# Performance work log

Hardware: AMD Instinct MI355X
Metric: run time of the kernel (lower is better)

Reference implementation:

```python
import jax, jax.numpy as jnp
import numpy as np

DIM = 96
HEADS = 3
HEAD_DIM = DIM // HEADS
WIN = (4, 4, 4)
N_WIN = WIN[0] * WIN[1] * WIN[2]  # 64 tokens per window
HIDDEN = int(DIM * 4.0)
EPS = 1e-5


def setup_inputs() -> dict:
    key = jax.random.key(0)
    ks = jax.random.split(key, 16)
    s = lambda fan: 1.0 / np.sqrt(fan)
    return {
        "x": jax.random.normal(ks[0], (1, 64, 96, 96, 96), jnp.float32),
        "g1": jnp.ones((DIM,), jnp.float32),
        "b1": jnp.zeros((DIM,), jnp.float32),
        "wq": jax.random.normal(ks[1], (DIM, DIM), jnp.float32) * s(DIM),
        "bq": jnp.zeros((DIM,), jnp.float32),
        "wkv": jax.random.normal(ks[2], (DIM, 2 * DIM), jnp.float32) * s(DIM),
        "bkv": jnp.zeros((2 * DIM,), jnp.float32),
        "wp": jax.random.normal(ks[3], (DIM, DIM), jnp.float32) * s(DIM),
        "bp": jnp.zeros((DIM,), jnp.float32),
        "g2": jnp.ones((DIM,), jnp.float32),
        "b2": jnp.zeros((DIM,), jnp.float32),
        "w1": jax.random.normal(ks[4], (DIM, HIDDEN), jnp.float32) * s(DIM),
        "bm1": jnp.zeros((HIDDEN,), jnp.float32),
        "w2": jax.random.normal(ks[5], (HIDDEN, DIM), jnp.float32) * s(HIDDEN),
        "bm2": jnp.zeros((DIM,), jnp.float32),
    }


def _layernorm(x, g, b):
    mu = jnp.mean(x, axis=-1, keepdims=True)
    var = jnp.mean(jnp.square(x - mu), axis=-1, keepdims=True)
    return (x - mu) * jax.lax.rsqrt(var + EPS) * g + b


def _window_partition(x):
    B, D, H, W, C = x.shape
    wd, wh, ww = WIN
    x = x.reshape(B, D // wd, wd, H // wh, wh, W // ww, ww, C)
    x = x.transpose(0, 1, 3, 5, 2, 4, 6, 7)
    return x.reshape(-1, N_WIN, C)


def _window_reverse(win, B, D, H, W):
    wd, wh, ww = WIN
    C = win.shape[-1]
    x = win.reshape(B, D // wd, H // wh, W // ww, wd, wh, ww, C)
    x = x.transpose(0, 1, 4, 2, 5, 3, 6, 7)
    return x.reshape(B, D, H, W, C)


def reference(x, g1, b1, wq, bq, wkv, bkv, wp, bp, g2, b2, w1, bm1, w2, bm2):
    B, D, H, W, C = x.shape
    # --- part 1: LN -> window attention -> residual ---
    h = _layernorm(x, g1, b1)
    # D,H,W chosen divisible by window size, so padding is a no-op
    xw = _window_partition(h)                       # (nW, N, C)
    nW = xw.shape[0]
    q = (xw @ wq + bq).reshape(nW, N_WIN, HEADS, HEAD_DIM)
    kv = (xw @ wkv + bkv).reshape(nW, N_WIN, 2, HEADS, HEAD_DIM)
    k, v = kv[:, :, 0], kv[:, :, 1]                 # (nW, N, h, hd)
    scale = HEAD_DIM ** -0.5
    attn = jnp.einsum("wnhd,wmhd->whnm", q * scale, k)
    attn = jax.nn.softmax(attn, axis=-1)
    out = jnp.einsum("whnm,wmhd->wnhd", attn, v).reshape(nW, N_WIN, C)
    out = out @ wp + bp
    attn_out = _window_reverse(out, B, D, H, W)
    x = x + attn_out
    # --- part 2: LN -> MLP -> residual ---
    h2 = _layernorm(x, g2, b2)
    h2 = jax.nn.gelu(h2 @ w1 + bm1, approximate=False) @ w2 + bm2
    return x + h2
```

## Files before the change

kernel.cpp:

```cpp
#include <hip/hip_runtime.h>

typedef __bf16 bf16x8 __attribute__((ext_vector_type(8)));
typedef __bf16 bf16x4 __attribute__((ext_vector_type(4)));
typedef float f32x4 __attribute__((ext_vector_type(4)));

#define MFMA(a,b,c) __builtin_amdgcn_mfma_f32_16x16x32_bf16(a, b, c, 0, 0, 0)

__device__ __forceinline__ float gelu_f(float t) {
    float t2 = t * t;
    float m = t * __builtin_fmaf(-0.07135481627f, t2, -1.5957691216f);
    float e = __expf(m);
    return t * __builtin_amdgcn_rcpf(1.0f + e);
}

__global__ void prep_weights(const float* __restrict__ wq, const float* __restrict__ wkv,
                             const float* __restrict__ wp, const float* __restrict__ w1,
                             const float* __restrict__ w2, __bf16* __restrict__ ws) {
    int i = blockIdx.x * 256 + threadIdx.x;
    const float scale = 0.17677669529663687f;
    if (i < 9216) {
        int n = i / 96, k = i % 96;
        ws[i] = (__bf16)(wq[k * 96 + n] * scale);
    } else if (i < 27648) {
        int j = i - 9216; int n = j / 96, k = j % 96;
        ws[i] = (__bf16)(wkv[k * 192 + n]);
    } else if (i < 36864) {
        int j = i - 27648; int n = j / 96, k = j % 96;
        ws[i] = (__bf16)(wp[k * 96 + n]);
    } else if (i < 73728) {
        int j = i - 36864; int n = j / 96, k = j % 96;
        ws[i] = (__bf16)(w1[k * 384 + n]);
    } else if (i < 110592) {
        int j = i - 73728; int n = j / 384, k = j % 384;
        ws[i] = (__bf16)(w2[k * 96 + n]);
    }
}

#define LDH 104

__global__ __launch_bounds__(256, 2) void attn_kernel(
    const float* __restrict__ x, const float* __restrict__ g1v, const float* __restrict__ b1v,
    const float* __restrict__ bq, const float* __restrict__ bkv, const float* __restrict__ bp,
    const __bf16* __restrict__ ws, float* __restrict__ xmid)
{
    const __bf16* wqt  = ws;
    const __bf16* wkvt = ws + 9216;
    const __bf16* wpt  = ws + 27648;

    __shared__ __align__(16) __bf16 h_lds[64 * LDH];
    __shared__ __align__(16) __bf16 q_lds[64 * LDH];
    __shared__ __align__(16) __bf16 k_lds[64 * LDH];
    __shared__ __align__(16) __bf16 vt_lds[96 * 72];
    __shared__ __align__(16) __bf16 p_lds[4 * 16 * 72];

    const int tid = threadIdx.x;
    const int wv = tid >> 6, lane = tid & 63;
    const int c = lane & 15, g = lane >> 4;
    const int mp = wv >> 1, ng = wv & 1;

    const int wid = blockIdx.x;
    const int wdI = wid / 576, rem = wid % 576, whI = rem / 24, wwI = rem % 24;
    const int tok = tid >> 2, cseg = (tid & 3) * 24;
    const int dz = tok >> 4, hy = (tok >> 2) & 3, wx = tok & 3;
    const long gbase = (((long)(wdI * 4 + dz) * 96 + (whI * 4 + hy)) * 96 + (wwI * 4 + wx)) * 96 + cseg;

    float xr[24];
    #pragma unroll
    for (int j = 0; j < 6; ++j) {
        float4 v = *reinterpret_cast<const float4*>(x + gbase + j * 4);
        xr[j*4+0] = v.x; xr[j*4+1] = v.y; xr[j*4+2] = v.z; xr[j*4+3] = v.w;
    }
    float s = 0.f;
    #pragma unroll
    for (int j = 0; j < 24; ++j) s += xr[j];
    s += __shfl_xor(s, 1); s += __shfl_xor(s, 2);
    float mu = s * (1.0f / 96.0f);
    float vs = 0.f;
    #pragma unroll
    for (int j = 0; j < 24; ++j) { float d = xr[j] - mu; vs += d * d; }
    vs += __shfl_xor(vs, 1); vs += __shfl_xor(vs, 2);
    float rstd = rsqrtf(vs * (1.0f / 96.0f) + 1e-5f);
    #pragma unroll
    for (int j = 0; j < 6; ++j) {
        float4 gv = *reinterpret_cast<const float4*>(g1v + cseg + j * 4);
        float4 bv = *reinterpret_cast<const float4*>(b1v + cseg + j * 4);
        h_lds[tok * LDH + cseg + j*4+0] = (__bf16)((xr[j*4+0] - mu) * rstd * gv.x + bv.x);
        h_lds[tok * LDH + cseg + j*4+1] = (__bf16)((xr[j*4+1] - mu) * rstd * gv.y + bv.y);
        h_lds[tok * LDH + cseg + j*4+2] = (__bf16)((xr[j*4+2] - mu) * rstd * gv.z + bv.z);
        h_lds[tok * LDH + cseg + j*4+3] = (__bf16)((xr[j*4+3] - mu) * rstd * gv.w + bv.w);
    }
    __syncthreads();

    {
        f32x4 acc[2][3];
        #pragma unroll
        for (int mi = 0; mi < 2; ++mi)
            #pragma unroll
            for (int nl = 0; nl < 3; ++nl) acc[mi][nl] = (f32x4){0.f, 0.f, 0.f, 0.f};
        #pragma unroll
        for (int kc = 0; kc < 3; ++kc) {
            bf16x8 a[2];
            #pragma unroll
            for (int mi = 0; mi < 2; ++mi)
                a[mi] = *reinterpret_cast<const bf16x8*>(&h_lds[((mp*2+mi)*16 + c) * LDH + kc*32 + g*8]);
            #pragma unroll
            for (int nl = 0; nl < 3; ++nl) {
                int nt = ng * 3 + nl;
                bf16x8 b = *reinterpret_cast<const bf16x8*>(&wqt[(nt*16 + c) * 96 + kc*32 + g*8]);
                #pragma unroll
                for (int mi = 0; mi < 2; ++mi)
                    acc[mi][nl] = MFMA(a[mi], b, acc[mi][nl]);
            }
        }
        #pragma unroll
        for (int nl = 0; nl < 3; ++nl) {
            int n = (ng * 3 + nl) * 16 + c;
            float bias = bq[n] * 0.17677669529663687f;
            #pragma unroll
            for (int mi = 0; mi < 2; ++mi)
                #pragma unroll
                for (int r = 0; r < 4; ++r)
                    q_lds[((mp*2+mi)*16 + g*4 + r) * LDH + n] = (__bf16)(acc[mi][nl][r] + bias);
        }
    }

    {
        f32x4 acc[4][3];
        #pragma unroll
        for (int m = 0; m < 4; ++m)
            #pragma unroll
            for (int nl = 0; nl < 3; ++nl) acc[m][nl] = (f32x4){0.f, 0.f, 0.f, 0.f};
        #pragma unroll
        for (int kc = 0; kc < 3; ++kc) {
            bf16x8 a[4];
            #pragma unroll
            for (int m = 0; m < 4; ++m)
                a[m] = *reinterpret_cast<const bf16x8*>(&h_lds[(m*16 + c) * LDH + kc*32 + g*8]);
            #pragma unroll
            for (int nl = 0; nl < 3; ++nl) {
                int nt = wv * 3 + nl;
                bf16x8 b = *reinterpret_cast<const bf16x8*>(&wkvt[(nt*16 + c) * 96 + kc*32 + g*8]);
                #pragma unroll
                for (int m = 0; m < 4; ++m)
                    acc[m][nl] = MFMA(a[m], b, acc[m][nl]);
            }
        }
        #pragma unroll
        for (int nl = 0; nl < 3; ++nl) {
            int n = (wv * 3 + nl) * 16 + c;
            float bias = bkv[n];
            if (wv < 2) {
                #pragma unroll
                for (int m = 0; m < 4; ++m)
                    #pragma unroll
                    for (int r = 0; r < 4; ++r)
                        k_lds[(m*16 + g*4 + r) * LDH + n] = (__bf16)(acc[m][nl][r] + bias);
            } else {
                int nv = n - 96;
                #pragma unroll
                for (int m = 0; m < 4; ++m) {
                    bf16x4 pk;
                    pk.x = (__bf16)(acc[m][nl][0] + bias);
                    pk.y = (__bf16)(acc[m][nl][1] + bias);
                    pk.z = (__bf16)(acc[m][nl][2] + bias);
                    pk.w = (__bf16)(acc[m][nl][3] + bias);
                    *reinterpret_cast<bf16x4*>(&vt_lds[nv * 72 + m*16 + g*4]) = pk;
                }
            }
        }
    }
    __syncthreads();

    __bf16* p_w = &p_lds[wv * (16 * 72)];
    #pragma unroll
    for (int h = 0; h < 3; ++h) {
        f32x4 sacc[4];
        #pragma unroll
        for (int nt = 0; nt < 4; ++nt) sacc[nt] = (f32x4){0.f, 0.f, 0.f, 0.f};
        bf16x8 a = *reinterpret_cast<const bf16x8*>(&q_lds[(wv*16 + c) * LDH + h*32 + g*8]);
        #pragma unroll
        for (int nt = 0; nt < 4; ++nt) {
            bf16x8 b = *reinterpret_cast<const bf16x8*>(&k_lds[(nt*16 + c) * LDH + h*32 + g*8]);
            sacc[nt] = MFMA(a, b, sacc[nt]);
        }
        float mx[4];
        #pragma unroll
        for (int r = 0; r < 4; ++r) {
            float m0 = fmaxf(fmaxf(sacc[0][r], sacc[1][r]), fmaxf(sacc[2][r], sacc[3][r]));
            m0 = fmaxf(m0, __shfl_xor(m0, 1));
            m0 = fmaxf(m0, __shfl_xor(m0, 2));
            m0 = fmaxf(m0, __shfl_xor(m0, 4));
            m0 = fmaxf(m0, __shfl_xor(m0, 8));
            mx[r] = m0;
        }
        float p[4][4];
        #pragma unroll
        for (int nt = 0; nt < 4; ++nt)
            #pragma unroll
            for (int r = 0; r < 4; ++r)
                p[nt][r] = __expf(sacc[nt][r] - mx[r]);
        float rsinv[4];
        #pragma unroll
        for (int r = 0; r < 4; ++r) {
            float s0 = p[0][r] + p[1][r] + p[2][r] + p[3][r];
            s0 += __shfl_xor(s0, 1); s0 += __shfl_xor(s0, 2);
            s0 += __shfl_xor(s0, 4); s0 += __shfl_xor(s0, 8);
            rsinv[r] = __builtin_amdgcn_rcpf(s0);
        }
        #pragma unroll
        for (int nt = 0; nt < 4; ++nt)
            #pragma unroll
            for (int r = 0; r < 4; ++r)
                p_w[(g*4 + r) * 72 + nt*16 + c] = (__bf16)p[nt][r];

        f32x4 oacc[2];
        oacc[0] = (f32x4){0.f, 0.f, 0.f, 0.f};
        oacc[1] = (f32x4){0.f, 0.f, 0.f, 0.f};
        #pragma unroll
        for (int kc = 0; kc < 2; ++kc) {
            bf16x8 pa = *reinterpret_cast<const bf16x8*>(&p_w[c * 72 + kc*32 + g*8]);
            #pragma unroll
            for (int n2 = 0; n2 < 2; ++n2) {
                bf16x8 b = *reinterpret_cast<const bf16x8*>(&vt_lds[(h*32 + n2*16 + c) * 72 + kc*32 + g*8]);
                oacc[n2] = MFMA(pa, b, oacc[n2]);
            }
        }
        #pragma unroll
        for (int n2 = 0; n2 < 2; ++n2)
            #pragma unroll
            for (int r = 0; r < 4; ++r)
                h_lds[(wv*16 + g*4 + r) * LDH + h*32 + n2*16 + c] = (__bf16)(oacc[n2][r] * rsinv[r]);
    }
    __syncthreads();

    {
        f32x4 acc[2][3];
        #pragma unroll
        for (int mi = 0; mi < 2; ++mi)
            #pragma unroll
            for (int nl = 0; nl < 3; ++nl) acc[mi][nl] = (f32x4){0.f, 0.f, 0.f, 0.f};
        #pragma unroll
        for (int kc = 0; kc < 3; ++kc) {
            bf16x8 a[2];
            #pragma unroll
            for (int mi = 0; mi < 2; ++mi)
                a[mi] = *reinterpret_cast<const bf16x8*>(&h_lds[((mp*2+mi)*16 + c) * LDH + kc*32 + g*8]);
            #pragma unroll
            for (int nl = 0; nl < 3; ++nl) {
                int nt = ng * 3 + nl;
                bf16x8 b = *reinterpret_cast<const bf16x8*>(&wpt[(nt*16 + c) * 96 + kc*32 + g*8]);
                #pragma unroll
                for (int mi = 0; mi < 2; ++mi)
                    acc[mi][nl] = MFMA(a[mi], b, acc[mi][nl]);
            }
        }
        __syncthreads();
        #pragma unroll
        for (int nl = 0; nl < 3; ++nl) {
            int n = (ng * 3 + nl) * 16 + c;
            float bias = bp[n];
            #pragma unroll
            for (int mi = 0; mi < 2; ++mi)
                #pragma unroll
                for (int r = 0; r < 4; ++r)
                    q_lds[((mp*2+mi)*16 + g*4 + r) * LDH + n] = (__bf16)(acc[mi][nl][r] + bias);
        }
    }
    __syncthreads();

    #pragma unroll
    for (int j = 0; j < 6; ++j) {
        float4 v;
        v.x = xr[j*4+0] + (float)q_lds[tok * LDH + cseg + j*4+0];
        v.y = xr[j*4+1] + (float)q_lds[tok * LDH + cseg + j*4+1];
        v.z = xr[j*4+2] + (float)q_lds[tok * LDH + cseg + j*4+2];
        v.w = xr[j*4+3] + (float)q_lds[tok * LDH + cseg + j*4+3];
        *reinterpret_cast<float4*>(xmid + gbase + j * 4) = v;
    }
}

#define LDU 104
#define LDCH 200

__global__ __launch_bounds__(384, 4) void mlp_kernel(
    float* __restrict__ xio, const float* __restrict__ g2v, const float* __restrict__ b2v,
    const float* __restrict__ bm1, const float* __restrict__ bm2,
    const __bf16* __restrict__ ws)
{
    const __bf16* w1t = ws + 36864;
    const __bf16* w2t = ws + 73728;

    __shared__ __align__(16) __bf16 u_lds[64 * LDU];
    __shared__ __align__(16) __bf16 hid[64 * LDCH];

    const int tid = threadIdx.x;
    const int wv = tid >> 6, lane = tid & 63;
    const int c = lane & 15, g = lane >> 4;

    const int tok = tid >> 2, cseg = (tid & 3) * 24;
    const long gaddr = ((long)blockIdx.x * 64 + tok) * 96 + cseg;

    const f32x4 fzero = {0.f, 0.f, 0.f, 0.f};

    if (tid < 256) {
        float xr[24];
        #pragma unroll
        for (int j = 0; j < 6; ++j) {
            float4 v = *reinterpret_cast<const float4*>(xio + gaddr + j * 4);
            xr[j*4+0] = v.x; xr[j*4+1] = v.y; xr[j*4+2] = v.z; xr[j*4+3] = v.w;
        }
        float s = 0.f;
        #pragma unroll
        for (int j = 0; j < 24; ++j) s += xr[j];
        s += __shfl_xor(s, 1); s += __shfl_xor(s, 2);
        float mu = s * (1.0f / 96.0f);
        float vs = 0.f;
        #pragma unroll
        for (int j = 0; j < 24; ++j) { float d = xr[j] - mu; vs += d * d; }
        vs += __shfl_xor(vs, 1); vs += __shfl_xor(vs, 2);
        float rstd = rsqrtf(vs * (1.0f / 96.0f) + 1e-5f);
        #pragma unroll
        for (int j = 0; j < 6; ++j) {
            f32x4 gv = *reinterpret_cast<const f32x4*>(g2v + cseg + j * 4);
            f32x4 bv = *reinterpret_cast<const f32x4*>(b2v + cseg + j * 4);
            bf16x4 o;
            #pragma unroll
            for (int r = 0; r < 4; ++r) o[r] = (__bf16)((xr[j*4+r] - mu) * rstd * gv[r] + bv[r]);
            *reinterpret_cast<bf16x4*>(&u_lds[tok * LDU + cseg + j*4]) = o;
        }
    }
    __syncthreads();

    f32x4 accB[4];
    #pragma unroll
    for (int tt = 0; tt < 4; ++tt) accB[tt] = fzero;

    #pragma unroll
    for (int chp = 0; chp < 2; ++chp) {
        bf16x8 aW2[6];
        #pragma unroll
        for (int kc2 = 0; kc2 < 6; ++kc2)
            aW2[kc2] = *reinterpret_cast<const bf16x8*>(&w2t[(wv*16 + c) * 384 + chp*192 + kc2*32 + g*8]);

        f32x4 accA0[4], accA1[4];
        #pragma unroll
        for (int tt = 0; tt < 4; ++tt) { accA0[tt] = fzero; accA1[tt] = fzero; }
        #pragma unroll
        for (int kc = 0; kc < 3; ++kc) {
            bf16x8 aW0 = *reinterpret_cast<const bf16x8*>(&w1t[((chp*12 + wv)*16 + c) * 96 + kc*32 + g*8]);
            bf16x8 aW1 = *reinterpret_cast<const bf16x8*>(&w1t[((chp*12 + 6 + wv)*16 + c) * 96 + kc*32 + g*8]);
            #pragma unroll
            for (int tt = 0; tt < 4; ++tt) {
                bf16x8 bU = *reinterpret_cast<const bf16x8*>(&u_lds[(tt*16 + c) * LDU + kc*32 + g*8]);
                accA0[tt] = MFMA(aW0, bU, accA0[tt]);
                accA1[tt] = MFMA(aW1, bU, accA1[tt]);
            }
        }
        {
            f32x4 bb0 = *reinterpret_cast<const f32x4*>(&bm1[(chp*12 + wv)*16 + 4*g]);
            f32x4 bb1 = *reinterpret_cast<const f32x4*>(&bm1[(chp*12 + 6 + wv)*16 + 4*g]);
            #pragma unroll
            for (int tt = 0; tt < 4; ++tt) {
                bf16x4 o0, o1;
                #pragma unroll
                for (int r = 0; r < 4; ++r) {
                    o0[r] = (__bf16)gelu_f(accA0[tt][r] + bb0[r]);
                    o1[r] = (__bf16)gelu_f(accA1[tt][r] + bb1[r]);
                }
                *reinterpret_cast<bf16x4*>(&hid[(tt*16 + c) * LDCH + wv*16 + 4*g]) = o0;
                *reinterpret_cast<bf16x4*>(&hid[(tt*16 + c) * LDCH + 96 + wv*16 + 4*g]) = o1;
            }
        }
        __syncthreads();

        #pragma unroll
        for (int kc2 = 0; kc2 < 6; ++kc2) {
            #pragma unroll
            for (int tt = 0; tt < 4; ++tt) {
                bf16x8 bHd = *reinterpret_cast<const bf16x8*>(&hid[(tt*16 + c) * LDCH + kc2*32 + g*8]);
                accB[tt] = MFMA(aW2[kc2], bHd, accB[tt]);
            }
        }
        if (chp == 0) __syncthreads();
    }

    {
        f32x4 bb = *reinterpret_cast<const f32x4*>(&bm2[wv*16 + 4*g]);
        #pragma unroll
        for (int tt = 0; tt < 4; ++tt) {
            bf16x4 o;
            #pragma unroll
            for (int r = 0; r < 4; ++r) o[r] = (__bf16)(accB[tt][r] + bb[r]);
            *reinterpret_cast<bf16x4*>(&u_lds[(tt*16 + c) * LDU + wv*16 + 4*g]) = o;
        }
    }
    __syncthreads();

    if (tid < 256) {
        #pragma unroll
        for (int j = 0; j < 6; ++j) {
            float4 xv = *reinterpret_cast<const float4*>(xio + gaddr + j * 4);
            bf16x4 mo = *reinterpret_cast<const bf16x4*>(&u_lds[tok * LDU + cseg + j*4]);
            float4 v;
            v.x = xv.x + (float)mo[0];
            v.y = xv.y + (float)mo[1];
            v.z = xv.z + (float)mo[2];
            v.w = xv.w + (float)mo[3];
            *reinterpret_cast<float4*>(xio + gaddr + j * 4) = v;
        }
    }
}

extern "C" void kernel_launch(void* const* d_in, const int* in_sizes, int n_in,
                              void* d_out, int out_size, void* d_ws, size_t ws_size,
                              hipStream_t stream) {
    (void)in_sizes; (void)n_in; (void)out_size; (void)ws_size;
    const float* x   = (const float*)d_in[0];
    const float* g1  = (const float*)d_in[1];
    const float* b1  = (const float*)d_in[2];
    const float* wq  = (const float*)d_in[3];
    const float* bq  = (const float*)d_in[4];
    const float* wkv = (const float*)d_in[5];
    const float* bkv = (const float*)d_in[6];
    const float* wp  = (const float*)d_in[7];
    const float* bp  = (const float*)d_in[8];
    const float* g2  = (const float*)d_in[9];
    const float* b2  = (const float*)d_in[10];
    const float* w1  = (const float*)d_in[11];
    const float* bm1 = (const float*)d_in[12];
    const float* w2  = (const float*)d_in[13];
    const float* bm2 = (const float*)d_in[14];
    float* out = (float*)d_out;
    __bf16* ws = (__bf16*)d_ws;

    prep_weights<<<432, 256, 0, stream>>>(wq, wkv, wp, w1, w2, ws);
    attn_kernel<<<9216, 256, 0, stream>>>(x, g1, b1, bq, bkv, bp, ws, out);
    mlp_kernel<<<9216, 384, 0, stream>>>(out, g2, b2, bm1, bm2, ws);
}
```

Before: 469.0 us.

## Use 512-thread blocks in attention kernel with redistributed wave work

Doubles the attention kernel's block from 4 to 8 waves and splits each GEMM (Q, K, V, projection) across 8 waves, giving each wave one 16-row tile and three column tiles. The 12 (query tile, head) pairs in the attention stage are spread unevenly: four waves handle two heads each and four handle one. LayerNorm and the residual writes use 8 threads per token and vectorised bf16x4 LDS stores and loads. The goal is more parallelism per window and a shorter serial chain per wave. In exchange, each block uses more LDS and registers, occupancy may drop, and the head split leaves waves unbalanced.

```diff
diff --git a/kernel.cpp b/kernel.cpp
--- a/kernel.cpp
+++ b/kernel.cpp
@@ -38,7 +38,7 @@
 
 #define LDH 104
 
-__global__ __launch_bounds__(256, 2) void attn_kernel(
+__global__ __launch_bounds__(512) void attn_kernel(
     const float* __restrict__ x, const float* __restrict__ g1v, const float* __restrict__ b1v,
     const float* __restrict__ bq, const float* __restrict__ bkv, const float* __restrict__ bp,
     const __bf16* __restrict__ ws, float* __restrict__ xmid)
@@ -51,230 +51,220 @@
     __shared__ __align__(16) __bf16 q_lds[64 * LDH];
     __shared__ __align__(16) __bf16 k_lds[64 * LDH];
     __shared__ __align__(16) __bf16 vt_lds[96 * 72];
-    __shared__ __align__(16) __bf16 p_lds[4 * 16 * 72];
+    __shared__ __align__(16) __bf16 p_lds[8 * 16 * 72];
 
     const int tid = threadIdx.x;
     const int wv = tid >> 6, lane = tid & 63;
     const int c = lane & 15, g = lane >> 4;
-    const int mp = wv >> 1, ng = wv & 1;
+    const int mq = wv >> 1, nh = wv & 1;
 
     const int wid = blockIdx.x;
     const int wdI = wid / 576, rem = wid % 576, whI = rem / 24, wwI = rem % 24;
-    const int tok = tid >> 2, cseg = (tid & 3) * 24;
+    const int tok = tid >> 3, cs = (tid & 7) * 12;
     const int dz = tok >> 4, hy = (tok >> 2) & 3, wx = tok & 3;
-    const long gbase = (((long)(wdI * 4 + dz) * 96 + (whI * 4 + hy)) * 96 + (wwI * 4 + wx)) * 96 + cseg;
-
-    float xr[24];
+    const long gbase = (((long)(wdI * 4 + dz) * 96 + (whI * 4 + hy)) * 96 + (wwI * 4 + wx)) * 96 + cs;
+
+    const f32x4 fzero = {0.f, 0.f, 0.f, 0.f};
+
+    float xr[12];
     #pragma unroll
-    for (int j = 0; j < 6; ++j) {
+    for (int j = 0; j < 3; ++j) {
         float4 v = *reinterpret_cast<const float4*>(x + gbase + j * 4);
         xr[j*4+0] = v.x; xr[j*4+1] = v.y; xr[j*4+2] = v.z; xr[j*4+3] = v.w;
     }
-    float s = 0.f;
-    #pragma unroll
-    for (int j = 0; j < 24; ++j) s += xr[j];
-    s += __shfl_xor(s, 1); s += __shfl_xor(s, 2);
-    float mu = s * (1.0f / 96.0f);
-    float vs = 0.f;
-    #pragma unroll
-    for (int j = 0; j < 24; ++j) { float d = xr[j] - mu; vs += d * d; }
-    vs += __shfl_xor(vs, 1); vs += __shfl_xor(vs, 2);
-    float rstd = rsqrtf(vs * (1.0f / 96.0f) + 1e-5f);
-    #pragma unroll
-    for (int j = 0; j < 6; ++j) {
-        float4 gv = *reinterpret_cast<const float4*>(g1v + cseg + j * 4);
-        float4 bv = *reinterpret_cast<const float4*>(b1v + cseg + j * 4);
-        h_lds[tok * LDH + cseg + j*4+0] = (__bf16)((xr[j*4+0] - mu) * rstd * gv.x + bv.x);
-        h_lds[tok * LDH + cseg + j*4+1] = (__bf16)((xr[j*4+1] - mu) * rstd * gv.y + bv.y);
-        h_lds[tok * LDH + cseg + j*4+2] = (__bf16)((xr[j*4+2] - mu) * rstd * gv.z + bv.z);
-        h_lds[tok * LDH + cseg + j*4+3] = (__bf16)((xr[j*4+3] - mu) * rstd * gv.w + bv.w);
-    }
-    __syncthreads();
-
-    {
-        f32x4 acc[2][3];
-        #pragma unroll
-        for (int mi = 0; mi < 2; ++mi)
-            #pragma unroll
-            for (int nl = 0; nl < 3; ++nl) acc[mi][nl] = (f32x4){0.f, 0.f, 0.f, 0.f};
+    {
+        float s = 0.f;
+        #pragma unroll
+        for (int j = 0; j < 12; ++j) s += xr[j];
+        s += __shfl_xor(s, 1); s += __shfl_xor(s, 2); s += __shfl_xor(s, 4);
+        float mu = s * (1.0f / 96.0f);
+        float vs = 0.f;
+        #pragma unroll
+        for (int j = 0; j < 12; ++j) { float d = xr[j] - mu; vs += d * d; }
+        vs += __shfl_xor(vs, 1); vs += __shfl_xor(vs, 2); vs += __shfl_xor(vs, 4);
+        float rstd = rsqrtf(vs * (1.0f / 96.0f) + 1e-5f);
+        #pragma unroll
+        for (int j = 0; j < 3; ++j) {
+            f32x4 gv = *reinterpret_cast<const f32x4*>(g1v + cs + j * 4);
+            f32x4 bv = *reinterpret_cast<const f32x4*>(b1v + cs + j * 4);
+            bf16x4 o;
+            #pragma unroll
+            for (int r = 0; r < 4; ++r) o[r] = (__bf16)((xr[j*4+r] - mu) * rstd * gv[r] + bv[r]);
+            *reinterpret_cast<bf16x4*>(&h_lds[tok * LDH + cs + j*4]) = o;
+        }
+    }
+    __syncthreads();
+
+    {
+        f32x4 acc[3];
+        #pragma unroll
+        for (int nl = 0; nl < 3; ++nl) acc[nl] = fzero;
         #pragma unroll
         for (int kc = 0; kc < 3; ++kc) {
-            bf16x8 a[2];
-            #pragma unroll
-            for (int mi = 0; mi < 2; ++mi)
-                a[mi] = *reinterpret_cast<const bf16x8*>(&h_lds[((mp*2+mi)*16 + c) * LDH + kc*32 + g*8]);
+            bf16x8 a = *reinterpret_cast<const bf16x8*>(&h_lds[(mq*16 + c) * LDH + kc*32 + g*8]);
             #pragma unroll
             for (int nl = 0; nl < 3; ++nl) {
-                int nt = ng * 3 + nl;
+                int nt = nh * 3 + nl;
                 bf16x8 b = *reinterpret_cast<const bf16x8*>(&wqt[(nt*16 + c) * 96 + kc*32 + g*8]);
-                #pragma unroll
-                for (int mi = 0; mi < 2; ++mi)
-                    acc[mi][nl] = MFMA(a[mi], b, acc[mi][nl]);
+                acc[nl] = MFMA(a, b, acc[nl]);
             }
         }
         #pragma unroll
         for (int nl = 0; nl < 3; ++nl) {
-            int n = (ng * 3 + nl) * 16 + c;
+            int n = (nh * 3 + nl) * 16 + c;
             float bias = bq[n] * 0.17677669529663687f;
             #pragma unroll
-            for (int mi = 0; mi < 2; ++mi)
+            for (int r = 0; r < 4; ++r)
+                q_lds[(mq*16 + g*4 + r) * LDH + n] = (__bf16)(acc[nl][r] + bias);
+        }
+    }
+    {
+        f32x4 acc[3];
+        #pragma unroll
+        for (int nl = 0; nl < 3; ++nl) acc[nl] = fzero;
+        #pragma unroll
+        for (int kc = 0; kc < 3; ++kc) {
+            bf16x8 a = *reinterpret_cast<const bf16x8*>(&h_lds[(mq*16 + c) * LDH + kc*32 + g*8]);
+            #pragma unroll
+            for (int nl = 0; nl < 3; ++nl) {
+                int nt = nh * 3 + nl;
+                bf16x8 b = *reinterpret_cast<const bf16x8*>(&wkvt[(nt*16 + c) * 96 + kc*32 + g*8]);
+                acc[nl] = MFMA(a, b, acc[nl]);
+            }
+        }
+        #pragma unroll
+        for (int nl = 0; nl < 3; ++nl) {
+            int n = (nh * 3 + nl) * 16 + c;
+            float bias = bkv[n];
+            #pragma unroll
+            for (int r = 0; r < 4; ++r)
+                k_lds[(mq*16 + g*4 + r) * LDH + n] = (__bf16)(acc[nl][r] + bias);
+        }
+    }
+    {
+        f32x4 av[3];
+        #pragma unroll
+        for (int nl = 0; nl < 3; ++nl) av[nl] = fzero;
+        #pragma unroll
+        for (int kc = 0; kc < 3; ++kc) {
+            bf16x8 aH = *reinterpret_cast<const bf16x8*>(&h_lds[(mq*16 + c) * LDH + kc*32 + g*8]);
+            #pragma unroll
+            for (int nl = 0; nl < 3; ++nl) {
+                int nv = nh * 3 + nl;
+                bf16x8 bW = *reinterpret_cast<const bf16x8*>(&wkvt[(96 + nv*16 + c) * 96 + kc*32 + g*8]);
+                av[nl] = MFMA(aH, bW, av[nl]);
+            }
+        }
+        #pragma unroll
+        for (int nl = 0; nl < 3; ++nl) {
+            int nv = nh * 3 + nl;
+            float bias = bkv[96 + nv*16 + c];
+            bf16x4 pk;
+            #pragma unroll
+            for (int r = 0; r < 4; ++r) pk[r] = (__bf16)(av[nl][r] + bias);
+            *reinterpret_cast<bf16x4*>(&vt_lds[(nv*16 + c) * 72 + mq*16 + g*4]) = pk;
+        }
+    }
+    __syncthreads();
+
+    {
+        const int qt = (wv < 4) ? wv : wv - 4;
+        const int nheads = (wv < 4) ? 2 : 1;
+        __bf16* p_w = &p_lds[wv * (16 * 72)];
+        for (int hi = 0; hi < nheads; ++hi) {
+            const int h = (wv < 4) ? (hi == 0 ? 0 : 2) : 1;
+            f32x4 sacc[4];
+            #pragma unroll
+            for (int nt = 0; nt < 4; ++nt) sacc[nt] = fzero;
+            bf16x8 a = *reinterpret_cast<const bf16x8*>(&q_lds[(qt*16 + c) * LDH + h*32 + g*8]);
+            #pragma unroll
+            for (int nt = 0; nt < 4; ++nt) {
+                bf16x8 b = *reinterpret_cast<const bf16x8*>(&k_lds[(nt*16 + c) * LDH + h*32 + g*8]);
+                sacc[nt] = MFMA(a, b, sacc[nt]);
+            }
+            float mx[4];
+            #pragma unroll
+            for (int r = 0; r < 4; ++r) {
+                float m0 = fmaxf(fmaxf(sacc[0][r], sacc[1][r]), fmaxf(sacc[2][r], sacc[3][r]));
+                m0 = fmaxf(m0, __shfl_xor(m0, 1));
+                m0 = fmaxf(m0, __shfl_xor(m0, 2));
+                m0 = fmaxf(m0, __shfl_xor(m0, 4));
+                m0 = fmaxf(m0, __shfl_xor(m0, 8));
+                mx[r] = m0;
+            }
+            float p[4][4];
+            #pragma unroll
+            for (int nt = 0; nt < 4; ++nt)
                 #pragma unroll
                 for (int r = 0; r < 4; ++r)
-                    q_lds[((mp*2+mi)*16 + g*4 + r) * LDH + n] = (__bf16)(acc[mi][nl][r] + bias);
-        }
-    }
-
-    {
-        f32x4 acc[4][3];
-        #pragma unroll
-        for (int m = 0; m < 4; ++m)
-            #pragma unroll
-            for (int nl = 0; nl < 3; ++nl) acc[m][nl] = (f32x4){0.f, 0.f, 0.f, 0.f};
-        #pragma unroll
-        for (int kc = 0; kc < 3; ++kc) {
-            bf16x8 a[4];
-            #pragma unroll
-            for (int m = 0; m < 4; ++m)
-                a[m] = *reinterpret_cast<const bf16x8*>(&h_lds[(m*16 + c) * LDH + kc*32 + g*8]);
-            #pragma unroll
-            for (int nl = 0; nl < 3; ++nl) {
-                int nt = wv * 3 + nl;
-                bf16x8 b = *reinterpret_cast<const bf16x8*>(&wkvt[(nt*16 + c) * 96 + kc*32 + g*8]);
-                #pragma unroll
-                for (int m = 0; m < 4; ++m)
-                    acc[m][nl] = MFMA(a[m], b, acc[m][nl]);
-            }
-        }
-        #pragma unroll
-        for (int nl = 0; nl < 3; ++nl) {
-            int n = (wv * 3 + nl) * 16 + c;
-            float bias = bkv[n];
-            if (wv < 2) {
-                #pragma unroll
-                for (int m = 0; m < 4; ++m)
-                    #pragma unroll
-                    for (int r = 0; r < 4; ++r)
-                        k_lds[(m*16 + g*4 + r) * LDH + n] = (__bf16)(acc[m][nl][r] + bias);
-            } else {
-                int nv = n - 96;
-                #pragma unroll
-                for (int m = 0; m < 4; ++m) {
-                    bf16x4 pk;
-                    pk.x = (__bf16)(acc[m][nl][0] + bias);
-                    pk.y = (__bf16)(acc[m][nl][1] + bias);
-                    pk.z = (__bf16)(acc[m][nl][2] + bias);
-                    pk.w = (__bf16)(acc[m][nl][3] + bias);
-                    *reinterpret_cast<bf16x4*>(&vt_lds[nv * 72 + m*16 + g*4]) = pk;
-                }
-            }
-        }
-    }
-    __syncthreads();
-
-    __bf16* p_w = &p_lds[wv * (16 * 72)];
-    #pragma unroll
-    for (int h = 0; h < 3; ++h) {
-        f32x4 sacc[4];
-        #pragma unroll
-        for (int nt = 0; nt < 4; ++nt) sacc[nt] = (f32x4){0.f, 0.f, 0.f, 0.f};
-        bf16x8 a = *reinterpret_cast<const bf16x8*>(&q_lds[(wv*16 + c) * LDH + h*32 + g*8]);
-        #pragma unroll
-        for (int nt = 0; nt < 4; ++nt) {
-            bf16x8 b = *reinterpret_cast<const bf16x8*>(&k_lds[(nt*16 + c) * LDH + h*32 + g*8]);
-            sacc[nt] = MFMA(a, b, sacc[nt]);
-        }
-        float mx[4];
-        #pragma unroll
-        for (int r = 0; r < 4; ++r) {
-            float m0 = fmaxf(fmaxf(sacc[0][r], sacc[1][r]), fmaxf(sacc[2][r], sacc[3][r]));
-            m0 = fmaxf(m0, __shfl_xor(m0, 1));
-            m0 = fmaxf(m0, __shfl_xor(m0, 2));
-            m0 = fmaxf(m0, __shfl_xor(m0, 4));
-            m0 = fmaxf(m0, __shfl_xor(m0, 8));
-            mx[r] = m0;
-        }
-        float p[4][4];
-        #pragma unroll
-        for (int nt = 0; nt < 4; ++nt)
-            #pragma unroll
-            for (int r = 0; r < 4; ++r)
-                p[nt][r] = __expf(sacc[nt][r] - mx[r]);
-        float rsinv[4];
-        #pragma unroll
-        for (int r = 0; r < 4; ++r) {
-            float s0 = p[0][r] + p[1][r] + p[2][r] + p[3][r];
-            s0 += __shfl_xor(s0, 1); s0 += __shfl_xor(s0, 2);
-            s0 += __shfl_xor(s0, 4); s0 += __shfl_xor(s0, 8);
-            rsinv[r] = __builtin_amdgcn_rcpf(s0);
-        }
-        #pragma unroll
-        for (int nt = 0; nt < 4; ++nt)
-            #pragma unroll
-            for (int r = 0; r < 4; ++r)
-                p_w[(g*4 + r) * 72 + nt*16 + c] = (__bf16)p[nt][r];
-
-        f32x4 oacc[2];
-        oacc[0] = (f32x4){0.f, 0.f, 0.f, 0.f};
-        oacc[1] = (f32x4){0.f, 0.f, 0.f, 0.f};
-        #pragma unroll
-        for (int kc = 0; kc < 2; ++kc) {
-            bf16x8 pa = *reinterpret_cast<const bf16x8*>(&p_w[c * 72 + kc*32 + g*8]);
-            #pragma unroll
-            for (int n2 = 0; n2 < 2; ++n2) {
-                bf16x8 b = *reinterpret_cast<const bf16x8*>(&vt_lds[(h*32 + n2*16 + c) * 72 + kc*32 + g*8]);
-                oacc[n2] = MFMA(pa, b, oacc[n2]);
-            }
-        }
-        #pragma unroll
-        for (int n2 = 0; n2 < 2; ++n2)
-            #pragma unroll
-            for (int r = 0; r < 4; ++r)
-                h_lds[(wv*16 + g*4 + r) * LDH + h*32 + n2*16 + c] = (__bf16)(oacc[n2][r] * rsinv[r]);
-    }
-    __syncthreads();
-
-    {
-        f32x4 acc[2][3];
-        #pragma unroll
-        for (int mi = 0; mi < 2; ++mi)
-            #pragma unroll
-            for (int nl = 0; nl < 3; ++nl) acc[mi][nl] = (f32x4){0.f, 0.f, 0.f, 0.f};
-        #pragma unroll
-        for (int kc = 0; kc < 3; ++kc) {
-            bf16x8 a[2];
-            #pragma unroll
-            for (int mi = 0; mi < 2; ++mi)
-                a[mi] = *reinterpret_cast<const bf16x8*>(&h_lds[((mp*2+mi)*16 + c) * LDH + kc*32 + g*8]);
-            #pragma unroll
-            for (int nl = 0; nl < 3; ++nl) {
-                int nt = ng * 3 + nl;
-                bf16x8 b = *reinterpret_cast<const bf16x8*>(&wpt[(nt*16 + c) * 96 + kc*32 + g*8]);
-                #pragma unroll
-                for (int mi = 0; mi < 2; ++mi)
-                    acc[mi][nl] = MFMA(a[mi], b, acc[mi][nl]);
-            }
-        }
-        __syncthreads();
-        #pragma unroll
-        for (int nl = 0; nl < 3; ++nl) {
-            int n = (ng * 3 + nl) * 16 + c;
-            float bias = bp[n];
-            #pragma unroll
-            for (int mi = 0; mi < 2; ++mi)
+                    p[nt][r] = __expf(sacc[nt][r] - mx[r]);
+            float rsinv[4];
+            #pragma unroll
+            for (int r = 0; r < 4; ++r) {
+                float s0 = p[0][r] + p[1][r] + p[2][r] + p[3][r];
+                s0 += __shfl_xor(s0, 1); s0 += __shfl_xor(s0, 2);
+                s0 += __shfl_xor(s0, 4); s0 += __shfl_xor(s0, 8);
+                rsinv[r] = __builtin_amdgcn_rcpf(s0);
+            }
+            #pragma unroll
+            for (int nt = 0; nt < 4; ++nt)
                 #pragma unroll
                 for (int r = 0; r < 4; ++r)
-                    q_lds[((mp*2+mi)*16 + g*4 + r) * LDH + n] = (__bf16)(acc[mi][nl][r] + bias);
+                    p_w[(g*4 + r) * 72 + nt*16 + c] = (__bf16)p[nt][r];
+
+            f32x4 oacc[2];
+            oacc[0] = fzero; oacc[1] = fzero;
+            #pragma unroll
+            for (int kc = 0; kc < 2; ++kc) {
+                bf16x8 pa = *reinterpret_cast<const bf16x8*>(&p_w[c * 72 + kc*32 + g*8]);
+                #pragma unroll
+                for (int n2 = 0; n2 < 2; ++n2) {
+                    bf16x8 b = *reinterpret_cast<const bf16x8*>(&vt_lds[(h*32 + n2*16 + c) * 72 + kc*32 + g*8]);
+                    oacc[n2] = MFMA(pa, b, oacc[n2]);
+                }
+            }
+            #pragma unroll
+            for (int n2 = 0; n2 < 2; ++n2)
+                #pragma unroll
+                for (int r = 0; r < 4; ++r)
+                    h_lds[(qt*16 + g*4 + r) * LDH + h*32 + n2*16 + c] = (__bf16)(oacc[n2][r] * rsinv[r]);
+        }
+    }
+    __syncthreads();
+
+    {
+        f32x4 acc[3];
+        #pragma unroll
+        for (int nl = 0; nl < 3; ++nl) acc[nl] = fzero;
+        #pragma unroll
+        for (int kc = 0; kc < 3; ++kc) {
+            bf16x8 a = *reinterpret_cast<const bf16x8*>(&h_lds[(mq*16 + c) * LDH + kc*32 + g*8]);
+            #pragma unroll
+            for (int nl = 0; nl < 3; ++nl) {
+                int nt = nh * 3 + nl;
+                bf16x8 b = *reinterpret_cast<const bf16x8*>(&wpt[(nt*16 + c) * 96 + kc*32 + g*8]);
+                acc[nl] = MFMA(a, b, acc[nl]);
+            }
+        }
+        #pragma unroll
+        for (int nl = 0; nl < 3; ++nl) {
+            int n = (nh * 3 + nl) * 16 + c;
+            float bias = bp[n];
+            #pragma unroll
+            for (int r = 0; r < 4; ++r)
+                q_lds[(mq*16 + g*4 + r) * LDH + n] = (__bf16)(acc[nl][r] + bias);
         }
     }
     __syncthreads();
 
     #pragma unroll
-    for (int j = 0; j < 6; ++j) {
+    for (int j = 0; j < 3; ++j) {
+        bf16x4 pr = *reinterpret_cast<const bf16x4*>(&q_lds[tok * LDH + cs + j*4]);
         float4 v;
-        v.x = xr[j*4+0] + (float)q_lds[tok * LDH + cseg + j*4+0];
-        v.y = xr[j*4+1] + (float)q_lds[tok * LDH + cseg + j*4+1];
-        v.z = xr[j*4+2] + (float)q_lds[tok * LDH + cseg + j*4+2];
-        v.w = xr[j*4+3] + (float)q_lds[tok * LDH + cseg + j*4+3];
+        v.x = xr[j*4+0] + (float)pr[0];
+        v.y = xr[j*4+1] + (float)pr[1];
+        v.z = xr[j*4+2] + (float)pr[2];
+        v.w = xr[j*4+3] + (float)pr[3];
         *reinterpret_cast<float4*>(xmid + gbase + j * 4) = v;
     }
 }
@@ -434,6 +424,6 @@
     __bf16* ws = (__bf16*)d_ws;
 
     prep_weights<<<432, 256, 0, stream>>>(wq, wkv, wp, w1, w2, ws);
-    attn_kernel<<<9216, 256, 0, stream>>>(x, g1, b1, bq, bkv, bp, ws, out);
+    attn_kernel<<<9216, 512, 0, stream>>>(x, g1, b1, bq, bkv, bp, ws, out);
     mlp_kernel<<<9216, 384, 0, stream>>>(out, g2, b2, bm1, bm2, ws);
 }
```

Result: slower. 589.6 us (+25.7%).
